# Kernel optimization log

Measured on AMD Instinct MI355X. Metric: run time of the kernel, lower is better.

## Reference

```python
import jax, jax.numpy as jnp
import numpy as np

DIM = 1024
CTX_DIM = 1024
HEADS = 16
HEAD_DIM = DIM // HEADS


def setup_inputs() -> dict:
    key = jax.random.key(0)
    ks = jax.random.split(key, 6)
    B, N, M = 2, 2048, 2048
    s = 0.02
    return {
        "x": jax.random.normal(ks[0], (B, N, DIM), dtype=jnp.float32),
        "context": jax.random.normal(ks[1], (B, M, CTX_DIM), dtype=jnp.float32),
        "W_q": jax.random.normal(ks[2], (DIM, DIM), dtype=jnp.float32) * s,
        "W_kv": jax.random.normal(ks[3], (CTX_DIM * 2, CTX_DIM), dtype=jnp.float32) * s,
        "W_proj": jax.random.normal(ks[4], (DIM, DIM), dtype=jnp.float32) * s,
        "b_proj": jax.random.normal(ks[5], (DIM,), dtype=jnp.float32) * s,
    }


def reference(x, context, W_q, W_kv, W_proj, b_proj):
    B, N, C = x.shape
    M = context.shape[1]
    scale = HEAD_DIM ** (-0.5)
    # q projection: [B,N,H,D]
    q = (x @ W_q.T).reshape(B, N, HEADS, HEAD_DIM) * scale
    # context kv projection: [B,M,2,H,D]
    kv = (context @ W_kv.T).reshape(B, M, 2, HEADS, HEAD_DIM)
    k = kv[:, :, 0]  # [B,M,H,D]
    v = kv[:, :, 0]  # NOTE: source uses qkv_context[0] for BOTH k and v (faithful)
    attn = jnp.einsum("bnhd,bmhd->bhnm", q, k)
    attn = jax.nn.softmax(attn, axis=-1)
    out = jnp.einsum("bhnm,bmhd->bnhd", attn, v).reshape(B, N, C)
    return out @ W_proj.T + b_proj
```

## Files before the change

kernel.cpp:

```cpp
#include <hip/hip_runtime.h>
#include <hip/hip_bf16.h>


typedef __bf16 bf16x8 __attribute__((ext_vector_type(8)));
typedef float f32x4 __attribute__((ext_vector_type(4)));
typedef float f32x16 __attribute__((ext_vector_type(16)));

static constexpr int kDIM = 1024;
static constexpr float kLog2e = 1.4426950408889634f;

__device__ inline unsigned short f2bf(float f) {
    union { float f; unsigned int u; } v; v.f = f;
    return (unsigned short)((v.u + 0x7FFFu + ((v.u >> 16) & 1u)) >> 16);
}

__device__ inline unsigned int pack2bf(float a, float b) {
    union { float f; unsigned int u; } ua, ub;
    ua.f = a; ub.f = b;
    return __builtin_amdgcn_perm(ub.u + 0x8000u, ua.u + 0x8000u, 0x07060302u);
}

__device__ inline void gload_lds16(const unsigned short* g, unsigned short* l) {
    __builtin_amdgcn_global_load_lds(
        (const __attribute__((address_space(1))) unsigned int*)g,
        (__attribute__((address_space(3))) unsigned int*)l, 16, 0, 0);
}

__global__ __launch_bounds__(256) void cast_all(
    const float* __restrict__ x, const float* __restrict__ ctx,
    const float* __restrict__ wq, const float* __restrict__ wkv,
    const float* __restrict__ wp,
    unsigned short* __restrict__ xb, unsigned short* __restrict__ cb,
    unsigned short* __restrict__ wqb, unsigned short* __restrict__ wkb,
    unsigned short* __restrict__ wpb)
{
    int j = blockIdx.x * 256 + threadIdx.x;
    const float* s; unsigned short* d;
    if (j < 1048576)                      { s = x;   d = xb;  }
    else if ((j -= 1048576) < 1048576)    { s = ctx; d = cb;  }
    else if ((j -= 1048576) < 262144)     { s = wq;  d = wqb; }
    else if ((j -= 262144) < 262144)      { s = wkv; d = wkb; }
    else if ((j -= 262144) < 262144)      { s = wp;  d = wpb; }
    else return;
    float4 f = ((const float4*)s)[j];
    ushort4 o;
    o.x = f2bf(f.x); o.y = f2bf(f.y); o.z = f2bf(f.z); o.w = f2bf(f.w);
    ((ushort4*)d)[j] = o;
}

__global__ __launch_bounds__(512) void gemm_qk(
    const unsigned short* __restrict__ xb, const unsigned short* __restrict__ cb,
    const unsigned short* __restrict__ Wq, const unsigned short* __restrict__ Wkv,
    unsigned short* __restrict__ Qb, unsigned short* __restrict__ Kb,
    unsigned short* __restrict__ Ktb, float qscale, int Mctx)
{
    __shared__ unsigned short As[128 * 64];
    __shared__ unsigned short Bs[128 * 64];
    const int z = blockIdx.z;
    const unsigned short* A  = z ? cb : xb;
    const unsigned short* Bw = z ? Wkv : Wq;
    unsigned short* Cb = z ? Kb : Qb;
    const float scale = z ? 1.0f : qscale;

    const int tid = threadIdx.x;
    const int wave = tid >> 6, lane = tid & 63;
    const int g = lane >> 4, c = lane & 15;
    const int wm = (wave & 1) * 64, wn = (wave >> 1) * 32;
    const int bm = blockIdx.y * 128, bn = blockIdx.x * 128;

    const int srow = lane >> 3, scol = (lane & 7) * 8;

    f32x4 acc[4][2];
    #pragma unroll
    for (int i = 0; i < 4; ++i)
        #pragma unroll
        for (int j = 0; j < 2; ++j)
            acc[i][j] = (f32x4){0.f, 0.f, 0.f, 0.f};

    for (int k0 = 0; k0 < kDIM; k0 += 64) {
        __syncthreads();
        #pragma unroll
        for (int t = 0; t < 2; ++t) {
            const int chunk = wave * 2 + t;
            const int row = chunk * 8 + srow;
            gload_lds16(A  + (size_t)(bm + row) * kDIM + k0 + scol, &As[chunk * 512]);
            gload_lds16(Bw + (size_t)(bn + row) * kDIM + k0 + scol, &Bs[chunk * 512]);
        }
        __syncthreads();
        #pragma unroll
        for (int kc = 0; kc < 2; ++kc) {
            bf16x8 af[4], bfr[2];
            #pragma unroll
            for (int i = 0; i < 4; ++i)
                af[i] = *(const bf16x8*)&As[(wm + i * 16 + c) * 64 + kc * 32 + g * 8];
            #pragma unroll
            for (int j = 0; j < 2; ++j)
                bfr[j] = *(const bf16x8*)&Bs[(wn + j * 16 + c) * 64 + kc * 32 + g * 8];
            #pragma unroll
            for (int i = 0; i < 4; ++i)
                #pragma unroll
                for (int j = 0; j < 2; ++j)
                    acc[i][j] = __builtin_amdgcn_mfma_f32_16x16x32_bf16(
                        af[i], bfr[j], acc[i][j], 0, 0, 0);
        }
    }

    #pragma unroll
    for (int i = 0; i < 4; ++i) {
        #pragma unroll
        for (int j = 0; j < 2; ++j) {
            const int r0 = bm + wm + i * 16 + 4 * g;
            const int cc = bn + wn + j * 16 + c;
            float v0 = acc[i][j][0] * scale;
            float v1 = acc[i][j][1] * scale;
            float v2 = acc[i][j][2] * scale;
            float v3 = acc[i][j][3] * scale;
            Cb[(size_t)(r0 + 0) * kDIM + cc] = f2bf(v0);
            Cb[(size_t)(r0 + 1) * kDIM + cc] = f2bf(v1);
            Cb[(size_t)(r0 + 2) * kDIM + cc] = f2bf(v2);
            Cb[(size_t)(r0 + 3) * kDIM + cc] = f2bf(v3);
            if (z) {
                const int bb = r0 / Mctx, n0 = r0 % Mctx;
                const int hh = cc >> 6, d = cc & 63;
                ushort4 pk;
                pk.x = f2bf(v0); pk.y = f2bf(v1); pk.z = f2bf(v2); pk.w = f2bf(v3);
                *(ushort4*)&Ktb[((size_t)((bb * 16 + hh) * 64 + d)) * Mctx + n0] = pk;
            }
        }
    }
}

__global__ __launch_bounds__(256) void gemm_proj(
    const unsigned short* __restrict__ Ab, const unsigned short* __restrict__ Wp,
    const float* __restrict__ bias, float* __restrict__ out)
{
    __shared__ unsigned short As[64 * 64];
    __shared__ unsigned short Bs[64 * 64];
    const int tid = threadIdx.x;
    const int wave = tid >> 6, lane = tid & 63;
    const int g = lane >> 4, c = lane & 15;
    const int wm = (wave & 1) * 32, wn = (wave >> 1) * 32;
    const int bm = blockIdx.y * 64, bn = blockIdx.x * 64;

    const int srow = lane >> 3, scol = (lane & 7) * 8;

    f32x4 acc[2][2];
    #pragma unroll
    for (int i = 0; i < 2; ++i)
        #pragma unroll
        for (int j = 0; j < 2; ++j)
            acc[i][j] = (f32x4){0.f, 0.f, 0.f, 0.f};

    for (int k0 = 0; k0 < kDIM; k0 += 64) {
        __syncthreads();
        #pragma unroll
        for (int t = 0; t < 2; ++t) {
            const int chunk = wave * 2 + t;
            const int row = chunk * 8 + srow;
            gload_lds16(Ab + (size_t)(bm + row) * kDIM + k0 + scol, &As[chunk * 512]);
            gload_lds16(Wp + (size_t)(bn + row) * kDIM + k0 + scol, &Bs[chunk * 512]);
        }
        __syncthreads();
        #pragma unroll
        for (int kc = 0; kc < 2; ++kc) {
            bf16x8 af[2], bfr[2];
            #pragma unroll
            for (int i = 0; i < 2; ++i)
                af[i] = *(const bf16x8*)&As[(wm + i * 16 + c) * 64 + kc * 32 + g * 8];
            #pragma unroll
            for (int j = 0; j < 2; ++j)
                bfr[j] = *(const bf16x8*)&Bs[(wn + j * 16 + c) * 64 + kc * 32 + g * 8];
            #pragma unroll
            for (int i = 0; i < 2; ++i)
                #pragma unroll
                for (int j = 0; j < 2; ++j)
                    acc[i][j] = __builtin_amdgcn_mfma_f32_16x16x32_bf16(
                        af[i], bfr[j], acc[i][j], 0, 0, 0);
        }
    }

    #pragma unroll
    for (int i = 0; i < 2; ++i) {
        #pragma unroll
        for (int j = 0; j < 2; ++j) {
            const int r0 = bm + wm + i * 16 + 4 * g;
            const int cc = bn + wn + j * 16 + c;
            const float bv = bias[cc];
            #pragma unroll
            for (int ii = 0; ii < 4; ++ii)
                out[(size_t)(r0 + ii) * kDIM + cc] = acc[i][j][ii] + bv;
        }
    }
}

__global__ __launch_bounds__(512, 4) void attn_mfma_v5(
    const unsigned short* __restrict__ Q,
    const unsigned short* __restrict__ K,
    const unsigned short* __restrict__ Kt,
    unsigned short* __restrict__ O, int N, int M)
{
    __shared__ unsigned short smem[18432];
    unsigned short* Ks  = smem;
    unsigned short* Kts = smem + 64 * 72;
    unsigned short* Ps  = smem + 2 * 64 * 72;

    const int b = blockIdx.z, h = blockIdx.y, q0 = blockIdx.x * 128;
    const int tid = threadIdx.x;
    const int w = tid >> 6, lane = tid & 63;
    const int strip = w >> 1, kh = w & 1;
    const int ql = lane & 31, l5 = lane >> 5;

    const unsigned short* Qrow = Q + (size_t)(b * N + q0 + strip * 32 + ql) * kDIM + h * 64;
    const unsigned short* Kb = K + (size_t)b * M * kDIM + h * 64;
    const unsigned short* Ktb = Kt + (size_t)((b * 16 + h) * 64) * M;

    bf16x8 bq[4];
    #pragma unroll
    for (int kc = 0; kc < 4; ++kc)
        bq[kc] = *(const bf16x8*)(Qrow + kc * 16 + l5 * 8);

    f32x16 ot[2];
    #pragma unroll
    for (int dt = 0; dt < 2; ++dt)
        #pragma unroll
        for (int r = 0; r < 16; ++r) ot[dt][r] = 0.f;
    float lac = 0.f;

    const int srow = tid >> 3, scol = (tid & 7) * 8;
    unsigned short* prow = &Ps[(strip * 32 + ql) * 72 + kh * 32];

    for (int k0 = 0; k0 < M; k0 += 64) {
        __syncthreads();
        *(uint4*)&Ks[srow * 72 + scol] =
            *(const uint4*)(Kb + (size_t)(k0 + srow) * kDIM + scol);
        *(uint4*)&Kts[srow * 72 + scol] =
            *(const uint4*)(Ktb + (size_t)srow * M + k0 + scol);
        __syncthreads();

        f32x16 st;
        #pragma unroll
        for (int r = 0; r < 16; ++r) st[r] = 0.f;
        #pragma unroll
        for (int kc = 0; kc < 4; ++kc) {
            bf16x8 ak = *(const bf16x8*)&Ks[(kh * 32 + ql) * 72 + kc * 16 + l5 * 8];
            st = __builtin_amdgcn_mfma_f32_32x32x16_bf16(ak, bq[kc], st, 0, 0, 0);
        }

        float pr[16];
        #pragma unroll
        for (int r = 0; r < 16; ++r) {
            pr[r] = __builtin_amdgcn_exp2f(st[r]);
            lac += pr[r];
        }
        unsigned int dw[8];
        #pragma unroll
        for (int p = 0; p < 8; ++p) dw[p] = pack2bf(pr[2 * p], pr[2 * p + 1]);
        #pragma unroll
        for (int pp = 0; pp < 4; ++pp)
            *(uint2*)&prow[8 * pp + 4 * l5] = make_uint2(dw[2 * pp], dw[2 * pp + 1]);

        #pragma unroll
        for (int kc2 = 0; kc2 < 2; ++kc2) {
            bf16x8 bp = *(const bf16x8*)&prow[kc2 * 16 + l5 * 8];
            #pragma unroll
            for (int dt = 0; dt < 2; ++dt) {
                bf16x8 av = *(const bf16x8*)&Kts[(dt * 32 + ql) * 72 + kh * 32 + kc2 * 16 + l5 * 8];
                ot[dt] = __builtin_amdgcn_mfma_f32_32x32x16_bf16(av, bp, ot[dt], 0, 0, 0);
            }
        }
    }

    float lw = lac + __shfl_xor(lac, 32);
    float* Om = (float*)smem;
    float* Lm = Om + 128 * 68;
    const int qi = strip * 32 + ql;

    __syncthreads();
    if (kh == 1) {
        #pragma unroll
        for (int dt = 0; dt < 2; ++dt)
            #pragma unroll
            for (int rr = 0; rr < 4; ++rr)
                *(f32x4*)&Om[qi * 68 + dt * 32 + 8 * rr + 4 * l5] =
                    (f32x4){ot[dt][4 * rr], ot[dt][4 * rr + 1],
                            ot[dt][4 * rr + 2], ot[dt][4 * rr + 3]};
        if (l5 == 0) Lm[qi] = lw;
    }
    __syncthreads();
    if (kh == 0) {
        const float inv = 1.0f / (lw + Lm[qi]);
        unsigned short* Ob = O + (size_t)(b * N + q0 + qi) * kDIM + h * 64;
        #pragma unroll
        for (int dt = 0; dt < 2; ++dt)
            #pragma unroll
            for (int rr = 0; rr < 4; ++rr) {
                f32x4 pv = *(const f32x4*)&Om[qi * 68 + dt * 32 + 8 * rr + 4 * l5];
                ushort4 u;
                u.x = f2bf((ot[dt][4 * rr]     + pv[0]) * inv);
                u.y = f2bf((ot[dt][4 * rr + 1] + pv[1]) * inv);
                u.z = f2bf((ot[dt][4 * rr + 2] + pv[2]) * inv);
                u.w = f2bf((ot[dt][4 * rr + 3] + pv[3]) * inv);
                *(ushort4*)(Ob + dt * 32 + 8 * rr + 4 * l5) = u;
            }
    }
}

extern "C" void kernel_launch(void* const* d_in, const int* in_sizes, int n_in,
                              void* d_out, int out_size, void* d_ws, size_t ws_size,
                              hipStream_t stream)
{
    const float* x      = (const float*)d_in[0];
    const float* ctxp   = (const float*)d_in[1];
    const float* W_q    = (const float*)d_in[2];
    const float* W_kv   = (const float*)d_in[3];
    const float* W_proj = (const float*)d_in[4];
    const float* b_proj = (const float*)d_in[5];
    float* out = (float*)d_out;

    const int B = 2, N = 2048, M = 2048;
    const int BN = B * N;
    const int SQ = kDIM * kDIM;

    unsigned short* p = (unsigned short*)d_ws;
    unsigned short* xb  = p; p += (size_t)BN * kDIM;
    unsigned short* cb  = p; p += (size_t)BN * kDIM;
    unsigned short* wqb = p; p += SQ;
    unsigned short* wkb = p; p += SQ;
    unsigned short* wpb = p; p += SQ;
    unsigned short* Qb  = p; p += (size_t)BN * kDIM;
    unsigned short* Kb  = p; p += (size_t)BN * kDIM;
    unsigned short* Ktb = p; p += (size_t)BN * kDIM;
    unsigned short* Ab  = xb;

    hipLaunchKernelGGL(cast_all, dim3(11264), dim3(256), 0, stream,
                       x, ctxp, W_q, W_kv, W_proj, xb, cb, wqb, wkb, wpb);
    hipLaunchKernelGGL(gemm_qk, dim3(kDIM / 128, BN / 128, 2), dim3(512), 0, stream,
                       xb, cb, wqb, wkb, Qb, Kb, Ktb, 0.125f * kLog2e, M);
    hipLaunchKernelGGL(attn_mfma_v5, dim3(N / 128, 16, B), dim3(512), 0, stream,
                       Qb, Kb, Ktb, Ab, N, M);
    hipLaunchKernelGGL(gemm_proj, dim3(kDIM / 64, BN / 64), dim3(256), 0, stream,
                       Ab, wpb, b_proj, out);
}
```

Before: 195.6 us.

## Shrink attention and QK GEMM tiles, pass P via lane shuffles, async K loads

The attention kernel now uses 64-query blocks of 4 waves instead of 128-query blocks of 8. It passes the bf16 probability fragments between lane halves with __shfl_xor rather than a round trip through LDS, and loads K and K-transposed tiles with global_load_lds, without padding, instead of through registers. The QK projection GEMM moves to 64-column tiles with 256 threads, and launch bounds are added for occupancy. The aim is less LDS traffic, fewer barriers and more resident blocks, at the cost of K tiles being reloaded once per 64 queries instead of once per 128, and possible LDS bank conflicts from the unpadded 64-element row stride.

```diff
diff --git a/kernel.cpp b/kernel.cpp
--- a/kernel.cpp
+++ b/kernel.cpp
@@ -48,14 +48,14 @@
     ((ushort4*)d)[j] = o;
 }
 
-__global__ __launch_bounds__(512) void gemm_qk(
+__global__ __launch_bounds__(256, 4) void gemm_qk(
     const unsigned short* __restrict__ xb, const unsigned short* __restrict__ cb,
     const unsigned short* __restrict__ Wq, const unsigned short* __restrict__ Wkv,
     unsigned short* __restrict__ Qb, unsigned short* __restrict__ Kb,
     unsigned short* __restrict__ Ktb, float qscale, int Mctx)
 {
     __shared__ unsigned short As[128 * 64];
-    __shared__ unsigned short Bs[128 * 64];
+    __shared__ unsigned short Bs[64 * 64];
     const int z = blockIdx.z;
     const unsigned short* A  = z ? cb : xb;
     const unsigned short* Bw = z ? Wkv : Wq;
@@ -66,7 +66,7 @@
     const int wave = tid >> 6, lane = tid & 63;
     const int g = lane >> 4, c = lane & 15;
     const int wm = (wave & 1) * 64, wn = (wave >> 1) * 32;
-    const int bm = blockIdx.y * 128, bn = blockIdx.x * 128;
+    const int bm = blockIdx.y * 128, bn = blockIdx.x * 64;
 
     const int srow = lane >> 3, scol = (lane & 7) * 8;
 
@@ -80,11 +80,16 @@
     for (int k0 = 0; k0 < kDIM; k0 += 64) {
         __syncthreads();
         #pragma unroll
+        for (int t = 0; t < 4; ++t) {
+            const int chunk = wave * 4 + t;
+            gload_lds16(A + (size_t)(bm + chunk * 8 + srow) * kDIM + k0 + scol,
+                        &As[chunk * 512]);
+        }
+        #pragma unroll
         for (int t = 0; t < 2; ++t) {
             const int chunk = wave * 2 + t;
-            const int row = chunk * 8 + srow;
-            gload_lds16(A  + (size_t)(bm + row) * kDIM + k0 + scol, &As[chunk * 512]);
-            gload_lds16(Bw + (size_t)(bn + row) * kDIM + k0 + scol, &Bs[chunk * 512]);
+            gload_lds16(Bw + (size_t)(bn + chunk * 8 + srow) * kDIM + k0 + scol,
+                        &Bs[chunk * 512]);
         }
         __syncthreads();
         #pragma unroll
@@ -130,7 +135,7 @@
     }
 }
 
-__global__ __launch_bounds__(256) void gemm_proj(
+__global__ __launch_bounds__(256, 4) void gemm_proj(
     const unsigned short* __restrict__ Ab, const unsigned short* __restrict__ Wp,
     const float* __restrict__ bias, float* __restrict__ out)
 {
@@ -193,22 +198,24 @@
     }
 }
 
-__global__ __launch_bounds__(512, 4) void attn_mfma_v5(
+__global__ __launch_bounds__(256, 4) void attn_mfma_v6(
     const unsigned short* __restrict__ Q,
     const unsigned short* __restrict__ K,
     const unsigned short* __restrict__ Kt,
     unsigned short* __restrict__ O, int N, int M)
 {
-    __shared__ unsigned short smem[18432];
-    unsigned short* Ks  = smem;
-    unsigned short* Kts = smem + 64 * 72;
-    unsigned short* Ps  = smem + 2 * 64 * 72;
-
-    const int b = blockIdx.z, h = blockIdx.y, q0 = blockIdx.x * 128;
+    __shared__ float smemf[64 * 68 + 64];
+    unsigned short* Ks  = (unsigned short*)smemf;
+    unsigned short* Kts = Ks + 64 * 64;
+    float* Om = smemf;
+    float* Lm = smemf + 64 * 68;
+
+    const int b = blockIdx.z, h = blockIdx.y, q0 = blockIdx.x * 64;
     const int tid = threadIdx.x;
     const int w = tid >> 6, lane = tid & 63;
     const int strip = w >> 1, kh = w & 1;
     const int ql = lane & 31, l5 = lane >> 5;
+    const int srow = lane >> 3, scol = (lane & 7) * 8;
 
     const unsigned short* Qrow = Q + (size_t)(b * N + q0 + strip * 32 + ql) * kDIM + h * 64;
     const unsigned short* Kb = K + (size_t)b * M * kDIM + h * 64;
@@ -226,15 +233,16 @@
         for (int r = 0; r < 16; ++r) ot[dt][r] = 0.f;
     float lac = 0.f;
 
-    const int srow = tid >> 3, scol = (tid & 7) * 8;
-    unsigned short* prow = &Ps[(strip * 32 + ql) * 72 + kh * 32];
-
     for (int k0 = 0; k0 < M; k0 += 64) {
         __syncthreads();
-        *(uint4*)&Ks[srow * 72 + scol] =
-            *(const uint4*)(Kb + (size_t)(k0 + srow) * kDIM + scol);
-        *(uint4*)&Kts[srow * 72 + scol] =
-            *(const uint4*)(Ktb + (size_t)srow * M + k0 + scol);
+        #pragma unroll
+        for (int t = 0; t < 2; ++t) {
+            const int chunk = w * 2 + t;
+            gload_lds16(Kb + (size_t)(k0 + chunk * 8 + srow) * kDIM + scol,
+                        &Ks[chunk * 512]);
+            gload_lds16(Ktb + (size_t)(chunk * 8 + srow) * M + k0 + scol,
+                        &Kts[chunk * 512]);
+        }
         __syncthreads();
 
         f32x16 st;
@@ -242,7 +250,7 @@
         for (int r = 0; r < 16; ++r) st[r] = 0.f;
         #pragma unroll
         for (int kc = 0; kc < 4; ++kc) {
-            bf16x8 ak = *(const bf16x8*)&Ks[(kh * 32 + ql) * 72 + kc * 16 + l5 * 8];
+            bf16x8 ak = *(const bf16x8*)&Ks[(kh * 32 + ql) * 64 + kc * 16 + l5 * 8];
             st = __builtin_amdgcn_mfma_f32_32x32x16_bf16(ak, bq[kc], st, 0, 0, 0);
         }
 
@@ -252,27 +260,34 @@
             pr[r] = __builtin_amdgcn_exp2f(st[r]);
             lac += pr[r];
         }
-        unsigned int dw[8];
+        unsigned int dw[8], ex[8];
         #pragma unroll
         for (int p = 0; p < 8; ++p) dw[p] = pack2bf(pr[2 * p], pr[2 * p + 1]);
         #pragma unroll
-        for (int pp = 0; pp < 4; ++pp)
-            *(uint2*)&prow[8 * pp + 4 * l5] = make_uint2(dw[2 * pp], dw[2 * pp + 1]);
+        for (int p = 0; p < 8; ++p) ex[p] = (unsigned int)__shfl_xor((int)dw[p], 32);
+        union FU { unsigned int u[4]; bf16x8 v; } bp0, bp1;
+        const bool hi = (l5 != 0);
+        bp0.u[0] = hi ? ex[2] : dw[0];
+        bp0.u[1] = hi ? ex[3] : dw[1];
+        bp0.u[2] = hi ? dw[2] : ex[0];
+        bp0.u[3] = hi ? dw[3] : ex[1];
+        bp1.u[0] = hi ? ex[6] : dw[4];
+        bp1.u[1] = hi ? ex[7] : dw[5];
+        bp1.u[2] = hi ? dw[6] : ex[4];
+        bp1.u[3] = hi ? dw[7] : ex[5];
 
         #pragma unroll
         for (int kc2 = 0; kc2 < 2; ++kc2) {
-            bf16x8 bp = *(const bf16x8*)&prow[kc2 * 16 + l5 * 8];
+            const bf16x8 bp = kc2 ? bp1.v : bp0.v;
             #pragma unroll
             for (int dt = 0; dt < 2; ++dt) {
-                bf16x8 av = *(const bf16x8*)&Kts[(dt * 32 + ql) * 72 + kh * 32 + kc2 * 16 + l5 * 8];
+                bf16x8 av = *(const bf16x8*)&Kts[(dt * 32 + ql) * 64 + kh * 32 + kc2 * 16 + l5 * 8];
                 ot[dt] = __builtin_amdgcn_mfma_f32_32x32x16_bf16(av, bp, ot[dt], 0, 0, 0);
             }
         }
     }
 
     float lw = lac + __shfl_xor(lac, 32);
-    float* Om = (float*)smem;
-    float* Lm = Om + 128 * 68;
     const int qi = strip * 32 + ql;
 
     __syncthreads();
@@ -334,9 +349,9 @@
 
     hipLaunchKernelGGL(cast_all, dim3(11264), dim3(256), 0, stream,
                        x, ctxp, W_q, W_kv, W_proj, xb, cb, wqb, wkb, wpb);
-    hipLaunchKernelGGL(gemm_qk, dim3(kDIM / 128, BN / 128, 2), dim3(512), 0, stream,
+    hipLaunchKernelGGL(gemm_qk, dim3(kDIM / 64, BN / 128, 2), dim3(256), 0, stream,
                        xb, cb, wqb, wkb, Qb, Kb, Ktb, 0.125f * kLog2e, M);
-    hipLaunchKernelGGL(attn_mfma_v5, dim3(N / 128, 16, B), dim3(512), 0, stream,
+    hipLaunchKernelGGL(attn_mfma_v6, dim3(N / 64, 16, B), dim3(256), 0, stream,
                        Qb, Kb, Ktb, Ab, N, M);
     hipLaunchKernelGGL(gemm_proj, dim3(kDIM / 64, BN / 64), dim3(256), 0, stream,
                        Ab, wpb, b_proj, out);
```

Result: slower. 233.3 us (+19.3%).

## Swizzle LDS tiles in QK/proj GEMMs and shrink QK block to 128x64

Applied to the files above, without the earlier changes.

Applies an XOR swizzle to the 16-byte column chunks written into LDS by global_load_lds and read back for MFMA fragments, in both the QK and output projection GEMMs, to cut LDS bank conflicts. The QK GEMM is also retiled from 512 threads with 128x128 tiles to 256 threads with 128x64 tiles, doubling the grid, with launch bounds requesting 4 blocks per CU. This trades fewer waves per block for more blocks and less LDS per block, which may change occupancy and reuse of A tiles.

```diff
diff --git a/kernel.cpp b/kernel.cpp
--- a/kernel.cpp
+++ b/kernel.cpp
@@ -48,14 +48,14 @@
     ((ushort4*)d)[j] = o;
 }
 
-__global__ __launch_bounds__(512) void gemm_qk(
+__global__ __launch_bounds__(256, 4) void gemm_qk(
     const unsigned short* __restrict__ xb, const unsigned short* __restrict__ cb,
     const unsigned short* __restrict__ Wq, const unsigned short* __restrict__ Wkv,
     unsigned short* __restrict__ Qb, unsigned short* __restrict__ Kb,
     unsigned short* __restrict__ Ktb, float qscale, int Mctx)
 {
     __shared__ unsigned short As[128 * 64];
-    __shared__ unsigned short Bs[128 * 64];
+    __shared__ unsigned short Bs[64 * 64];
     const int z = blockIdx.z;
     const unsigned short* A  = z ? cb : xb;
     const unsigned short* Bw = z ? Wkv : Wq;
@@ -66,9 +66,11 @@
     const int wave = tid >> 6, lane = tid & 63;
     const int g = lane >> 4, c = lane & 15;
     const int wm = (wave & 1) * 64, wn = (wave >> 1) * 32;
-    const int bm = blockIdx.y * 128, bn = blockIdx.x * 128;
-
-    const int srow = lane >> 3, scol = (lane & 7) * 8;
+    const int bm = blockIdx.y * 128, bn = blockIdx.x * 64;
+
+    const int srow = lane >> 3;
+    const int scolsw = ((lane & 7) ^ (srow & 7)) * 8;
+    const int x7 = c & 7;
 
     f32x4 acc[4][2];
     #pragma unroll
@@ -80,11 +82,16 @@
     for (int k0 = 0; k0 < kDIM; k0 += 64) {
         __syncthreads();
         #pragma unroll
+        for (int t = 0; t < 4; ++t) {
+            const int chunk = wave * 4 + t;
+            gload_lds16(A + (size_t)(bm + chunk * 8 + srow) * kDIM + k0 + scolsw,
+                        &As[chunk * 512]);
+        }
+        #pragma unroll
         for (int t = 0; t < 2; ++t) {
             const int chunk = wave * 2 + t;
-            const int row = chunk * 8 + srow;
-            gload_lds16(A  + (size_t)(bm + row) * kDIM + k0 + scol, &As[chunk * 512]);
-            gload_lds16(Bw + (size_t)(bn + row) * kDIM + k0 + scol, &Bs[chunk * 512]);
+            gload_lds16(Bw + (size_t)(bn + chunk * 8 + srow) * kDIM + k0 + scolsw,
+                        &Bs[chunk * 512]);
         }
         __syncthreads();
         #pragma unroll
@@ -92,10 +99,12 @@
             bf16x8 af[4], bfr[2];
             #pragma unroll
             for (int i = 0; i < 4; ++i)
-                af[i] = *(const bf16x8*)&As[(wm + i * 16 + c) * 64 + kc * 32 + g * 8];
+                af[i] = *(const bf16x8*)&As[(wm + i * 16 + c) * 64 +
+                                            ((kc * 4 + g) ^ x7) * 8];
             #pragma unroll
             for (int j = 0; j < 2; ++j)
-                bfr[j] = *(const bf16x8*)&Bs[(wn + j * 16 + c) * 64 + kc * 32 + g * 8];
+                bfr[j] = *(const bf16x8*)&Bs[(wn + j * 16 + c) * 64 +
+                                             ((kc * 4 + g) ^ x7) * 8];
             #pragma unroll
             for (int i = 0; i < 4; ++i)
                 #pragma unroll
@@ -130,7 +139,7 @@
     }
 }
 
-__global__ __launch_bounds__(256) void gemm_proj(
+__global__ __launch_bounds__(256, 4) void gemm_proj(
     const unsigned short* __restrict__ Ab, const unsigned short* __restrict__ Wp,
     const float* __restrict__ bias, float* __restrict__ out)
 {
@@ -142,7 +151,9 @@
     const int wm = (wave & 1) * 32, wn = (wave >> 1) * 32;
     const int bm = blockIdx.y * 64, bn = blockIdx.x * 64;
 
-    const int srow = lane >> 3, scol = (lane & 7) * 8;
+    const int srow = lane >> 3;
+    const int scolsw = ((lane & 7) ^ (srow & 7)) * 8;
+    const int x7 = c & 7;
 
     f32x4 acc[2][2];
     #pragma unroll
@@ -157,8 +168,8 @@
         for (int t = 0; t < 2; ++t) {
             const int chunk = wave * 2 + t;
             const int row = chunk * 8 + srow;
-            gload_lds16(Ab + (size_t)(bm + row) * kDIM + k0 + scol, &As[chunk * 512]);
-            gload_lds16(Wp + (size_t)(bn + row) * kDIM + k0 + scol, &Bs[chunk * 512]);
+            gload_lds16(Ab + (size_t)(bm + row) * kDIM + k0 + scolsw, &As[chunk * 512]);
+            gload_lds16(Wp + (size_t)(bn + row) * kDIM + k0 + scolsw, &Bs[chunk * 512]);
         }
         __syncthreads();
         #pragma unroll
@@ -166,10 +177,12 @@
             bf16x8 af[2], bfr[2];
             #pragma unroll
             for (int i = 0; i < 2; ++i)
-                af[i] = *(const bf16x8*)&As[(wm + i * 16 + c) * 64 + kc * 32 + g * 8];
+                af[i] = *(const bf16x8*)&As[(wm + i * 16 + c) * 64 +
+                                            ((kc * 4 + g) ^ x7) * 8];
             #pragma unroll
             for (int j = 0; j < 2; ++j)
-                bfr[j] = *(const bf16x8*)&Bs[(wn + j * 16 + c) * 64 + kc * 32 + g * 8];
+                bfr[j] = *(const bf16x8*)&Bs[(wn + j * 16 + c) * 64 +
+                                             ((kc * 4 + g) ^ x7) * 8];
             #pragma unroll
             for (int i = 0; i < 2; ++i)
                 #pragma unroll
@@ -334,7 +347,7 @@
 
     hipLaunchKernelGGL(cast_all, dim3(11264), dim3(256), 0, stream,
                        x, ctxp, W_q, W_kv, W_proj, xb, cb, wqb, wkb, wpb);
-    hipLaunchKernelGGL(gemm_qk, dim3(kDIM / 128, BN / 128, 2), dim3(512), 0, stream,
+    hipLaunchKernelGGL(gemm_qk, dim3(kDIM / 64, BN / 128, 2), dim3(256), 0, stream,
                        xb, cb, wqb, wkb, Qb, Kb, Ktb, 0.125f * kLog2e, M);
     hipLaunchKernelGGL(attn_mfma_v5, dim3(N / 128, 16, B), dim3(512), 0, stream,
                        Qb, Kb, Ktb, Ab, N, M);
```

Measured after the change: 190.9 us. -2.4%, faster.
